# Kernel optimization log

Measured on AMD Instinct MI355X. Metric: run time of the kernel, lower is better.

The kernel has to match this reference:

```python
import jax, jax.numpy as jnp
import numpy as np

S, B, D, V = 1024, 8, 512, 8000


def _ln(x, g, b, eps=1e-5):
    m = x.mean(-1, keepdims=True)
    v = x.var(-1, keepdims=True)
    return (x - m) / jnp.sqrt(v + eps) * g + b


def setup_inputs() -> dict:
    key = jax.random.key(0)
    ks = jax.random.split(key, 8)
    representation = jax.random.normal(ks[0], (S, B, D), jnp.float32)
    # CTC-style logits: tokens come in runs of ~4 frames so argmax has segments
    tok = jax.random.randint(ks[1], (S // 4, B), 0, V)
    tok = jnp.repeat(tok, 4, axis=0)  # [S,B]
    logit = jax.random.normal(ks[2], (S, B, V), jnp.float32) + 6.0 * jax.nn.one_hot(tok, V, dtype=jnp.float32)
    padding = jnp.zeros((B, S), bool)  # all frames valid
    # linear_adapter: Linear(D,2D) -> ReLU -> Linear(2D,D) -> LayerNorm
    w1 = jax.random.normal(ks[3], (2 * D, D), jnp.float32) * (D ** -0.5)
    b1 = jnp.zeros((2 * D,), jnp.float32)
    w2 = jax.random.normal(ks[4], (D, 2 * D), jnp.float32) * ((2 * D) ** -0.5)
    b2 = jnp.zeros((D,), jnp.float32)
    ln1_g = jnp.ones((D,), jnp.float32)
    ln1_b = jnp.zeros((D,), jnp.float32)
    # embed_adapter weight [dict_size, dim], init std = dim**-0.5
    emb_w = jax.random.normal(ks[5], (V, D), jnp.float32) * (D ** -0.5)
    eln_g = jnp.ones((D,), jnp.float32)
    eln_b = jnp.zeros((D,), jnp.float32)
    return dict(representation=representation, logit=logit, padding=padding,
                w1=w1, b1=b1, w2=w2, b2=b2, ln1_g=ln1_g, ln1_b=ln1_b,
                emb_w=emb_w, eln_g=eln_g, eln_b=eln_b)


def reference(representation, logit, padding, w1, b1, w2, b2, ln1_g, ln1_b, emb_w, eln_g, eln_b):
    # distribution = softmax(logit / T), T = 1.0
    dist = jax.nn.softmax(logit, axis=-1)  # [S,B,V]
    # linear adapter: Linear -> ReLU -> Linear -> LN
    h = jax.nn.relu(jnp.einsum('sbd,ed->sbe', representation, w1) + b1)
    linear_out = _ln(jnp.einsum('sbe,de->sbd', h, w2) + b2, ln1_g, ln1_b)
    # context adapter: dist @ embed_adapter.weight, then embed LN
    soft_out = _ln(jnp.einsum('sbv,vd->sbd', dist, emb_w), eln_g, eln_b)
    out = linear_out + soft_out  # league
    # --- CTC 'avg' compress (shrink), vectorized; output padded to S frames ---
    pred = jnp.argmax(dist, axis=-1).T  # [B,S]
    valid = ~padding  # [B,S]
    prev = jnp.concatenate([jnp.full((pred.shape[0], 1), -1, pred.dtype), pred[:, :-1]], axis=1)
    change = (pred != prev) & valid  # segment starts
    seg = jnp.cumsum(change, axis=1) - 1  # segment id per frame
    seg = jnp.where(valid, seg, S)  # invalid frames -> out-of-range id
    # weights_matrix[b, t, s] = 1/len(segment s) if frame t in segment s
    onehot = (seg[:, :, None] == jnp.arange(S)[None, None, :]).astype(out.dtype)  # [B,S,S]
    counts = onehot.sum(1)  # [B,S] frames per segment
    w = onehot * jnp.where(counts > 0, 1.0 / counts, 0.0)[:, None, :]
    # representation.permute(1,2,0).bmm(weights).permute(2,0,1)
    compressed = jnp.einsum('sbd,bst->tbd', out, w)  # [S_new(padded to S), B, D]
    new_lengths = change.sum(1)
    new_padding = jnp.arange(S)[None, :] >= new_lengths[:, None]
    return compressed, new_padding
```

## Files before the change

kernel.cpp:

```cpp
#include <hip/hip_runtime.h>
#include <hip/hip_bf16.h>

typedef __attribute__((ext_vector_type(8))) __bf16 bf16x8;
typedef __attribute__((ext_vector_type(4))) __bf16 bf16x4;
typedef __attribute__((ext_vector_type(4))) float  f32x4;

#define AS1 __attribute__((address_space(1)))
#define AS3 __attribute__((address_space(3)))

__global__ __launch_bounds__(256) void k_cvt(const float* __restrict__ in,
                                             __bf16* __restrict__ out, int n4) {
  int i = blockIdx.x * 256 + threadIdx.x;
  if (i >= n4) return;
  float4 f = reinterpret_cast<const float4*>(in)[i];
  bf16x4 o = { (__bf16)f.x, (__bf16)f.y, (__bf16)f.z, (__bf16)f.w };
  reinterpret_cast<bf16x4*>(out)[i] = o;
}

__global__ __launch_bounds__(256) void k_transpose_cvt(const float* __restrict__ in,
                                                       __bf16* __restrict__ out) {
  __shared__ float t[32][33];
  int bi = blockIdx.x, bj = blockIdx.y;
  int c = threadIdx.x & 31, r8 = threadIdx.x >> 5;
#pragma unroll
  for (int i = 0; i < 4; ++i) {
    int r = r8 + i * 8;
    t[r][c] = in[(size_t)(bi * 32 + r) * 512 + bj * 32 + c];
  }
  __syncthreads();
#pragma unroll
  for (int i = 0; i < 4; ++i) {
    int r = r8 + i * 8;
    out[(size_t)(bj * 32 + r) * 8000 + bi * 32 + c] = (__bf16)t[c][r];
  }
}

__global__ __launch_bounds__(256) void k_softmax(const float* __restrict__ logit,
                                                 __bf16* __restrict__ dist,
                                                 int* __restrict__ pred) {
  int row = blockIdx.x, tid = threadIdx.x;
  int lane = tid & 63, wid = tid >> 6;
  const float4* lr = (const float4*)(logit + (size_t)row * 8000);
  float4 v[8];
  float lmax = -1e30f; int lidx = 0;
#pragma unroll
  for (int j = 0; j < 8; ++j) {
    int i4 = tid + j * 256;
    if (i4 < 2000) v[j] = lr[i4];
    else { v[j].x = v[j].y = v[j].z = v[j].w = -1e30f; }
#pragma unroll
    for (int c = 0; c < 4; ++c) {
      float x = (&v[j].x)[c];
      if (x > lmax) { lmax = x; lidx = i4 * 4 + c; }
    }
  }
#pragma unroll
  for (int o = 32; o; o >>= 1) {
    float ov = __shfl_xor(lmax, o);
    int   oi = __shfl_xor(lidx, o);
    if (ov > lmax || (ov == lmax && oi < lidx)) { lmax = ov; lidx = oi; }
  }
  __shared__ float wmax[4]; __shared__ int widx[4]; __shared__ float wsum[4];
  if (lane == 0) { wmax[wid] = lmax; widx[wid] = lidx; }
  __syncthreads();
  float gmax = wmax[0]; int gidx = widx[0];
#pragma unroll
  for (int w = 1; w < 4; ++w)
    if (wmax[w] > gmax || (wmax[w] == gmax && widx[w] < gidx)) { gmax = wmax[w]; gidx = widx[w]; }
  float ls = 0.f;
#pragma unroll
  for (int j = 0; j < 8; ++j) {
#pragma unroll
    for (int c = 0; c < 4; ++c) {
      float e = __expf((&v[j].x)[c] - gmax);
      (&v[j].x)[c] = e; ls += e;
    }
  }
#pragma unroll
  for (int o = 32; o; o >>= 1) ls += __shfl_xor(ls, o);
  if (lane == 0) wsum[wid] = ls;
  __syncthreads();
  float inv = 1.f / (wsum[0] + wsum[1] + wsum[2] + wsum[3]);
  bf16x4* dr = (bf16x4*)(dist + (size_t)row * 8000);
#pragma unroll
  for (int j = 0; j < 8; ++j) {
    int i4 = tid + j * 256;
    if (i4 < 2000) {
      bf16x4 o = { (__bf16)(v[j].x * inv), (__bf16)(v[j].y * inv),
                   (__bf16)(v[j].z * inv), (__bf16)(v[j].w * inv) };
      dr[i4] = o;
    }
  }
  if (tid == 0) pred[row] = gidx;
}

template<int EPI>
__global__ __launch_bounds__(256) void k_gemm_bt(const __bf16* __restrict__ A,
                                                 const __bf16* __restrict__ B,
                                                 float* __restrict__ Cf,
                                                 __bf16* __restrict__ Cb,
                                                 const float* __restrict__ bias,
                                                 int K, int N, int klen, long long ostride) {
  __shared__ __align__(16) __bf16 lA[2][128 * 64];
  __shared__ __align__(16) __bf16 lB[2][128 * 64];
  int tid = threadIdx.x, lane = tid & 63, wid = tid >> 6;
  int wr = wid >> 1, wc = wid & 1;
  int k0 = blockIdx.z * klen;
  int kn = min(klen, K - k0);
  int nt = kn >> 6;
  const __bf16* Ab = A + (size_t)blockIdx.x * 128 * K + k0;
  const __bf16* Bb = B + (size_t)blockIdx.y * 128 * K + k0;
  int sr = tid >> 3, ss = tid & 7;
  f32x4 acc[4][4] = {};

  auto stage = [&](int buf, int kt) {
#pragma unroll
    for (int i = 0; i < 4; ++i) {
      int r = i * 32 + sr;
      int col = kt + ((ss ^ (r & 7)) << 3);
      __builtin_amdgcn_global_load_lds((const AS1 void*)(Ab + (size_t)r * K + col),
                                       (AS3 void*)(&lA[buf][i * 2048 + tid * 8]), 16, 0, 0);
      __builtin_amdgcn_global_load_lds((const AS1 void*)(Bb + (size_t)r * K + col),
                                       (AS3 void*)(&lB[buf][i * 2048 + tid * 8]), 16, 0, 0);
    }
  };

  stage(0, 0);
  __syncthreads();
  int cur = 0;
  for (int t = 0; t < nt; ++t) {
    if (t + 1 < nt) stage(cur ^ 1, (t + 1) << 6);
#pragma unroll
    for (int kk = 0; kk < 2; ++kk) {
      bf16x8 af[4], bv[4];
#pragma unroll
      for (int m = 0; m < 4; ++m) {
        int r = wr * 64 + m * 16 + (lane & 15);
        int slot = ((kk << 2) + (lane >> 4)) ^ (r & 7);
        af[m] = *(const bf16x8*)((const char*)lA[cur] + r * 128 + slot * 16);
      }
#pragma unroll
      for (int n = 0; n < 4; ++n) {
        int r = wc * 64 + n * 16 + (lane & 15);
        int slot = ((kk << 2) + (lane >> 4)) ^ (r & 7);
        bv[n] = *(const bf16x8*)((const char*)lB[cur] + r * 128 + slot * 16);
      }
#pragma unroll
      for (int m = 0; m < 4; ++m)
#pragma unroll
        for (int n = 0; n < 4; ++n)
          acc[m][n] = __builtin_amdgcn_mfma_f32_16x16x32_bf16(af[m], bv[n], acc[m][n], 0, 0, 0);
    }
    __syncthreads();
    cur ^= 1;
  }
  if (EPI == 0) Cf += (size_t)blockIdx.z * (size_t)ostride;
  int row0 = blockIdx.x * 128 + wr * 64 + ((lane >> 4) << 2);
  int col0 = blockIdx.y * 128 + wc * 64 + (lane & 15);
#pragma unroll
  for (int n = 0; n < 4; ++n) {
    int col = col0 + n * 16;
    float bvv = (EPI >= 1) ? bias[col] : 0.f;
#pragma unroll
    for (int m = 0; m < 4; ++m) {
#pragma unroll
      for (int j = 0; j < 4; ++j) {
        int row = row0 + m * 16 + j;
        float val = acc[m][n][j] + bvv;
        if (EPI == 1) { val = fmaxf(val, 0.f); Cb[(size_t)row * N + col] = (__bf16)val; }
        else          { Cf[(size_t)row * N + col] = val; }
      }
    }
  }
}

__global__ __launch_bounds__(256) void k_lnadd(const float* __restrict__ lin,
                                               const float* __restrict__ s0p,
                                               const float* __restrict__ s1p,
                                               const float* __restrict__ g1, const float* __restrict__ b1,
                                               const float* __restrict__ g2, const float* __restrict__ b2,
                                               float* __restrict__ out) {
  int wid = threadIdx.x >> 6, lane = threadIdx.x & 63;
  int row = blockIdx.x * 4 + wid;
  size_t base = (size_t)row * 512 + lane * 8;
  f32x4 a0 = *(const f32x4*)(lin + base), a1 = *(const f32x4*)(lin + base + 4);
  f32x4 c0 = *(const f32x4*)(s0p + base), c1 = *(const f32x4*)(s0p + base + 4);
  f32x4 d0 = *(const f32x4*)(s1p + base), d1 = *(const f32x4*)(s1p + base + 4);
  float x[8], y[8];
#pragma unroll
  for (int k = 0; k < 4; ++k) {
    x[k] = a0[k]; x[k + 4] = a1[k];
    y[k] = c0[k] + d0[k]; y[k + 4] = c1[k] + d1[k];
  }
  float sx = 0, qx = 0, sy = 0, qy = 0;
#pragma unroll
  for (int k = 0; k < 8; ++k) { sx += x[k]; qx += x[k] * x[k]; sy += y[k]; qy += y[k] * y[k]; }
#pragma unroll
  for (int o = 32; o; o >>= 1) {
    sx += __shfl_xor(sx, o); qx += __shfl_xor(qx, o);
    sy += __shfl_xor(sy, o); qy += __shfl_xor(qy, o);
  }
  const float invD = 1.f / 512.f;
  float mx = sx * invD, vx = qx * invD - mx * mx;
  float my = sy * invD, vy = qy * invD - my * my;
  float rx = rsqrtf(vx + 1e-5f), ry = rsqrtf(vy + 1e-5f);
  float o8[8];
#pragma unroll
  for (int k = 0; k < 8; ++k) {
    int d = lane * 8 + k;
    o8[k] = (x[k] - mx) * rx * g1[d] + b1[d] + (y[k] - my) * ry * g2[d] + b2[d];
  }
  *(f32x4*)(out + base)     = f32x4{o8[0], o8[1], o8[2], o8[3]};
  *(f32x4*)(out + base + 4) = f32x4{o8[4], o8[5], o8[6], o8[7]};
}

__global__ __launch_bounds__(256) void k_scan(const int* __restrict__ pred,
                                              int* __restrict__ seg_start,
                                              int* __restrict__ seg_cnt,
                                              int* __restrict__ new_len,
                                              float* __restrict__ out_pad) {
  __shared__ int lp[8192];
  __shared__ int len_s[8];
  int tid = threadIdx.x;
  for (int i = tid; i < 8192; i += 256) lp[i] = pred[i];
  __syncthreads();
  if (tid < 8) {
    int b = tid, prev = -1, seg = -1, start = 0;
    for (int s = 0; s < 1024; ++s) {
      int p = lp[s * 8 + b];
      if (p != prev) {
        if (seg >= 0) seg_cnt[b * 1024 + seg] = s - start;
        ++seg; seg_start[b * 1024 + seg] = s; start = s; prev = p;
      }
    }
    seg_cnt[b * 1024 + seg] = 1024 - start;
    len_s[b] = seg + 1;
    new_len[b] = seg + 1;
  }
  __syncthreads();
  for (int i = tid; i < 8192; i += 256) {
    int b = i >> 10, s = i & 1023;
    out_pad[b * 1024 + s] = (s >= len_s[b]) ? 1.f : 0.f;
  }
}

__global__ __launch_bounds__(256) void k_compress(const float* __restrict__ outb,
                                                  const int* __restrict__ seg_start,
                                                  const int* __restrict__ seg_cnt,
                                                  const int* __restrict__ new_len,
                                                  float* __restrict__ comp) {
  int wid = threadIdx.x >> 6, lane = threadIdx.x & 63;
  int t = blockIdx.x * 4 + wid, b = blockIdx.y;
  float* dst = comp + ((size_t)(t * 8 + b)) * 512 + lane * 8;
  int len = new_len[b];
  if (t >= len) {
    f32x4 z = {0.f, 0.f, 0.f, 0.f};
    *(f32x4*)dst = z; *(f32x4*)(dst + 4) = z;
    return;
  }
  int s0 = seg_start[b * 1024 + t], cnt = seg_cnt[b * 1024 + t];
  f32x4 a0 = {0.f, 0.f, 0.f, 0.f}, a1 = {0.f, 0.f, 0.f, 0.f};
  for (int s = s0; s < s0 + cnt; ++s) {
    const float* p = outb + ((size_t)(s * 8 + b)) * 512 + lane * 8;
    a0 += *(const f32x4*)p;
    a1 += *(const f32x4*)(p + 4);
  }
  float inv = 1.f / (float)cnt;
  a0 *= inv; a1 *= inv;
  *(f32x4*)dst = a0; *(f32x4*)(dst + 4) = a1;
}

extern "C" void kernel_launch(void* const* d_in, const int* in_sizes, int n_in,
                              void* d_out, int out_size, void* d_ws, size_t ws_size,
                              hipStream_t stream) {
  const float* rep   = (const float*)d_in[0];
  const float* logit = (const float*)d_in[1];
  const float* w1    = (const float*)d_in[3];
  const float* b1    = (const float*)d_in[4];
  const float* w2    = (const float*)d_in[5];
  const float* b2    = (const float*)d_in[6];
  const float* g1    = (const float*)d_in[7];
  const float* bb1   = (const float*)d_in[8];
  const float* emb   = (const float*)d_in[9];
  const float* g2    = (const float*)d_in[10];
  const float* bb2   = (const float*)d_in[11];
  float* out = (float*)d_out;
  (void)in_sizes; (void)n_in; (void)out_size; (void)ws_size;

  char* ws = (char*)d_ws;
  size_t off = 0;
  auto alloc = [&](size_t bytes) -> void* {
    void* p = ws + off; off += (bytes + 255) & ~(size_t)255; return p;
  };
  __bf16* Xb    = (__bf16*)alloc((size_t)8192 * 512 * 2);
  __bf16* w1b   = (__bf16*)alloc((size_t)1024 * 512 * 2);
  __bf16* w2b   = (__bf16*)alloc((size_t)512 * 1024 * 2);
  __bf16* embT  = (__bf16*)alloc((size_t)512 * 8000 * 2);
  __bf16* distb = (__bf16*)alloc((size_t)8192 * 8000 * 2);
  __bf16* Hb    = (__bf16*)alloc((size_t)8192 * 1024 * 2);
  float*  linr  = (float*)alloc((size_t)8192 * 512 * 4);
  float*  sof0  = (float*)alloc((size_t)8192 * 512 * 4 * 2);
  float*  sof1  = sof0 + (size_t)8192 * 512;
  float*  outb  = (float*)alloc((size_t)8192 * 512 * 4);
  int*    pred  = (int*)alloc((size_t)8192 * 4);
  int*    segs  = (int*)alloc((size_t)8192 * 4);
  int*    segc  = (int*)alloc((size_t)8192 * 4);
  int*    nlen  = (int*)alloc(64);

  k_cvt<<<4096, 256, 0, stream>>>(rep, Xb, 1048576);
  k_cvt<<<512, 256, 0, stream>>>(w1, w1b, 131072);
  k_cvt<<<512, 256, 0, stream>>>(w2, w2b, 131072);
  k_transpose_cvt<<<dim3(250, 16), 256, 0, stream>>>(emb, embT);
  k_softmax<<<8192, 256, 0, stream>>>(logit, distb, pred);
  k_gemm_bt<1><<<dim3(64, 8, 1), 256, 0, stream>>>(Xb, w1b, nullptr, Hb, b1, 512, 1024, 512, 0);
  k_gemm_bt<2><<<dim3(64, 4, 1), 256, 0, stream>>>(Hb, w2b, linr, nullptr, b2, 1024, 512, 1024, 0);
  k_gemm_bt<0><<<dim3(64, 4, 2), 256, 0, stream>>>(distb, embT, sof0, nullptr, nullptr,
                                                   8000, 512, 4096, (long long)8192 * 512);
  k_lnadd<<<2048, 256, 0, stream>>>(linr, sof0, sof1, g1, bb1, g2, bb2, outb);
  k_scan<<<1, 256, 0, stream>>>(pred, segs, segc, nlen, out + (size_t)8192 * 512);
  k_compress<<<dim3(256, 8), 256, 0, stream>>>(outb, segs, segc, nlen, out);
}
```

Baseline: 327.1 us.

## Triple-buffer GEMM loads, emit bf16 split-K partials, fuse prep kernels

```diff
diff --git a/kernel.cpp b/kernel.cpp
--- a/kernel.cpp
+++ b/kernel.cpp
@@ -8,30 +8,39 @@
 #define AS1 __attribute__((address_space(1)))
 #define AS3 __attribute__((address_space(3)))
 
-__global__ __launch_bounds__(256) void k_cvt(const float* __restrict__ in,
-                                             __bf16* __restrict__ out, int n4) {
-  int i = blockIdx.x * 256 + threadIdx.x;
-  if (i >= n4) return;
-  float4 f = reinterpret_cast<const float4*>(in)[i];
-  bf16x4 o = { (__bf16)f.x, (__bf16)f.y, (__bf16)f.z, (__bf16)f.w };
-  reinterpret_cast<bf16x4*>(out)[i] = o;
-}
-
-__global__ __launch_bounds__(256) void k_transpose_cvt(const float* __restrict__ in,
-                                                       __bf16* __restrict__ out) {
+__global__ __launch_bounds__(256) void k_prep(const float* __restrict__ rep,
+                                              const float* __restrict__ w1,
+                                              const float* __restrict__ w2,
+                                              const float* __restrict__ emb,
+                                              __bf16* __restrict__ Xb,
+                                              __bf16* __restrict__ w1b,
+                                              __bf16* __restrict__ w2b,
+                                              __bf16* __restrict__ embT) {
   __shared__ float t[32][33];
-  int bi = blockIdx.x, bj = blockIdx.y;
-  int c = threadIdx.x & 31, r8 = threadIdx.x >> 5;
-#pragma unroll
-  for (int i = 0; i < 4; ++i) {
-    int r = r8 + i * 8;
-    t[r][c] = in[(size_t)(bi * 32 + r) * 512 + bj * 32 + c];
-  }
-  __syncthreads();
-#pragma unroll
-  for (int i = 0; i < 4; ++i) {
-    int r = r8 + i * 8;
-    out[(size_t)(bj * 32 + r) * 8000 + bi * 32 + c] = (__bf16)t[c][r];
+  int bid = blockIdx.x;
+  if (bid < 5120) {
+    const float* in; __bf16* out; int i;
+    if (bid < 4096)      { in = rep; out = Xb;  i = bid * 256 + threadIdx.x; }
+    else if (bid < 4608) { in = w1;  out = w1b; i = (bid - 4096) * 256 + threadIdx.x; }
+    else                 { in = w2;  out = w2b; i = (bid - 4608) * 256 + threadIdx.x; }
+    float4 f = reinterpret_cast<const float4*>(in)[i];
+    bf16x4 o = { (__bf16)f.x, (__bf16)f.y, (__bf16)f.z, (__bf16)f.w };
+    reinterpret_cast<bf16x4*>(out)[i] = o;
+  } else {
+    int b2 = bid - 5120;
+    int bi = b2 % 250, bj = b2 / 250;
+    int c = threadIdx.x & 31, r8 = threadIdx.x >> 5;
+#pragma unroll
+    for (int i = 0; i < 4; ++i) {
+      int r = r8 + i * 8;
+      t[r][c] = emb[(size_t)(bi * 32 + r) * 512 + bj * 32 + c];
+    }
+    __syncthreads();
+#pragma unroll
+    for (int i = 0; i < 4; ++i) {
+      int r = r8 + i * 8;
+      embT[(size_t)(bj * 32 + r) * 8000 + bi * 32 + c] = (__bf16)t[c][r];
+    }
   }
 }
 
@@ -97,12 +106,11 @@
 template<int EPI>
 __global__ __launch_bounds__(256) void k_gemm_bt(const __bf16* __restrict__ A,
                                                  const __bf16* __restrict__ B,
-                                                 float* __restrict__ Cf,
                                                  __bf16* __restrict__ Cb,
                                                  const float* __restrict__ bias,
                                                  int K, int N, int klen, long long ostride) {
-  __shared__ __align__(16) __bf16 lA[2][128 * 64];
-  __shared__ __align__(16) __bf16 lB[2][128 * 64];
+  __shared__ __align__(16) __bf16 lA[3][128 * 64];
+  __shared__ __align__(16) __bf16 lB[3][128 * 64];
   int tid = threadIdx.x, lane = tid & 63, wid = tid >> 6;
   int wr = wid >> 1, wc = wid & 1;
   int k0 = blockIdx.z * klen;
@@ -117,7 +125,7 @@
 #pragma unroll
     for (int i = 0; i < 4; ++i) {
       int r = i * 32 + sr;
-      int col = kt + ((ss ^ (r & 7)) << 3);
+      int col = (kt << 6) + ((ss ^ (r & 7)) << 3);
       __builtin_amdgcn_global_load_lds((const AS1 void*)(Ab + (size_t)r * K + col),
                                        (AS3 void*)(&lA[buf][i * 2048 + tid * 8]), 16, 0, 0);
       __builtin_amdgcn_global_load_lds((const AS1 void*)(Bb + (size_t)r * K + col),
@@ -126,10 +134,18 @@
   };
 
   stage(0, 0);
-  __syncthreads();
-  int cur = 0;
+  if (nt > 1) stage(1, 1);
   for (int t = 0; t < nt; ++t) {
-    if (t + 1 < nt) stage(cur ^ 1, (t + 1) << 6);
+    int b = t % 3;
+    if (t + 2 < nt) {
+      stage((t + 2) % 3, t + 2);
+      asm volatile("s_waitcnt vmcnt(16)" ::: "memory");
+    } else if (t + 1 < nt) {
+      asm volatile("s_waitcnt vmcnt(8)" ::: "memory");
+    } else {
+      asm volatile("s_waitcnt vmcnt(0)" ::: "memory");
+    }
+    __builtin_amdgcn_s_barrier();
 #pragma unroll
     for (int kk = 0; kk < 2; ++kk) {
       bf16x8 af[4], bv[4];
@@ -137,13 +153,13 @@
       for (int m = 0; m < 4; ++m) {
         int r = wr * 64 + m * 16 + (lane & 15);
         int slot = ((kk << 2) + (lane >> 4)) ^ (r & 7);
-        af[m] = *(const bf16x8*)((const char*)lA[cur] + r * 128 + slot * 16);
+        af[m] = *(const bf16x8*)((const char*)lA[b] + r * 128 + slot * 16);
       }
 #pragma unroll
       for (int n = 0; n < 4; ++n) {
         int r = wc * 64 + n * 16 + (lane & 15);
         int slot = ((kk << 2) + (lane >> 4)) ^ (r & 7);
-        bv[n] = *(const bf16x8*)((const char*)lB[cur] + r * 128 + slot * 16);
+        bv[n] = *(const bf16x8*)((const char*)lB[b] + r * 128 + slot * 16);
       }
 #pragma unroll
       for (int m = 0; m < 4; ++m)
@@ -151,46 +167,47 @@
         for (int n = 0; n < 4; ++n)
           acc[m][n] = __builtin_amdgcn_mfma_f32_16x16x32_bf16(af[m], bv[n], acc[m][n], 0, 0, 0);
     }
-    __syncthreads();
-    cur ^= 1;
-  }
-  if (EPI == 0) Cf += (size_t)blockIdx.z * (size_t)ostride;
+    __builtin_amdgcn_s_barrier();
+  }
+  if (EPI == 0) Cb += (size_t)blockIdx.z * (size_t)ostride;
   int row0 = blockIdx.x * 128 + wr * 64 + ((lane >> 4) << 2);
   int col0 = blockIdx.y * 128 + wc * 64 + (lane & 15);
 #pragma unroll
   for (int n = 0; n < 4; ++n) {
     int col = col0 + n * 16;
-    float bvv = (EPI >= 1) ? bias[col] : 0.f;
+    float bvv = (EPI == 1) ? bias[col] : 0.f;
 #pragma unroll
     for (int m = 0; m < 4; ++m) {
 #pragma unroll
       for (int j = 0; j < 4; ++j) {
         int row = row0 + m * 16 + j;
         float val = acc[m][n][j] + bvv;
-        if (EPI == 1) { val = fmaxf(val, 0.f); Cb[(size_t)row * N + col] = (__bf16)val; }
-        else          { Cf[(size_t)row * N + col] = val; }
+        if (EPI == 1) val = fmaxf(val, 0.f);
+        Cb[(size_t)row * N + col] = (__bf16)val;
       }
     }
   }
 }
 
-__global__ __launch_bounds__(256) void k_lnadd(const float* __restrict__ lin,
-                                               const float* __restrict__ s0p,
-                                               const float* __restrict__ s1p,
+__global__ __launch_bounds__(256) void k_lnadd(const __bf16* __restrict__ lin,
+                                               const __bf16* __restrict__ sof,
+                                               const float* __restrict__ bias2,
                                                const float* __restrict__ g1, const float* __restrict__ b1,
                                                const float* __restrict__ g2, const float* __restrict__ b2,
                                                float* __restrict__ out) {
+  const long long P = (long long)8192 * 512;
   int wid = threadIdx.x >> 6, lane = threadIdx.x & 63;
   int row = blockIdx.x * 4 + wid;
   size_t base = (size_t)row * 512 + lane * 8;
-  f32x4 a0 = *(const f32x4*)(lin + base), a1 = *(const f32x4*)(lin + base + 4);
-  f32x4 c0 = *(const f32x4*)(s0p + base), c1 = *(const f32x4*)(s0p + base + 4);
-  f32x4 d0 = *(const f32x4*)(s1p + base), d1 = *(const f32x4*)(s1p + base + 4);
+  bf16x8 l0 = *(const bf16x8*)(lin + base);
+  bf16x8 l1 = *(const bf16x8*)(lin + P + base);
+  bf16x8 s0 = *(const bf16x8*)(sof + base);
+  bf16x8 s1 = *(const bf16x8*)(sof + P + base);
   float x[8], y[8];
 #pragma unroll
-  for (int k = 0; k < 4; ++k) {
-    x[k] = a0[k]; x[k + 4] = a1[k];
-    y[k] = c0[k] + d0[k]; y[k + 4] = c1[k] + d1[k];
+  for (int k = 0; k < 8; ++k) {
+    x[k] = (float)l0[k] + (float)l1[k] + bias2[lane * 8 + k];
+    y[k] = (float)s0[k] + (float)s1[k];
   }
   float sx = 0, qx = 0, sy = 0, qy = 0;
 #pragma unroll
@@ -222,12 +239,13 @@
   __shared__ int lp[8192];
   __shared__ int len_s[8];
   int tid = threadIdx.x;
-  for (int i = tid; i < 8192; i += 256) lp[i] = pred[i];
+  for (int i = tid; i < 8192; i += 256) lp[(i & 7) * 1024 + (i >> 3)] = pred[i];
   __syncthreads();
   if (tid < 8) {
     int b = tid, prev = -1, seg = -1, start = 0;
+    const int* row = lp + b * 1024;
     for (int s = 0; s < 1024; ++s) {
-      int p = lp[s * 8 + b];
+      int p = row[s];
       if (p != prev) {
         if (seg >= 0) seg_cnt[b * 1024 + seg] = s - start;
         ++seg; seg_start[b * 1024 + seg] = s; start = s; prev = p;
@@ -292,31 +310,27 @@
   auto alloc = [&](size_t bytes) -> void* {
     void* p = ws + off; off += (bytes + 255) & ~(size_t)255; return p;
   };
-  __bf16* Xb    = (__bf16*)alloc((size_t)8192 * 512 * 2);
+  const long long P = (long long)8192 * 512;
+  __bf16* Xb    = (__bf16*)alloc((size_t)P * 2);
   __bf16* w1b   = (__bf16*)alloc((size_t)1024 * 512 * 2);
   __bf16* w2b   = (__bf16*)alloc((size_t)512 * 1024 * 2);
   __bf16* embT  = (__bf16*)alloc((size_t)512 * 8000 * 2);
   __bf16* distb = (__bf16*)alloc((size_t)8192 * 8000 * 2);
   __bf16* Hb    = (__bf16*)alloc((size_t)8192 * 1024 * 2);
-  float*  linr  = (float*)alloc((size_t)8192 * 512 * 4);
-  float*  sof0  = (float*)alloc((size_t)8192 * 512 * 4 * 2);
-  float*  sof1  = sof0 + (size_t)8192 * 512;
-  float*  outb  = (float*)alloc((size_t)8192 * 512 * 4);
+  __bf16* linp  = (__bf16*)alloc((size_t)P * 2 * 2);
+  __bf16* sofp  = (__bf16*)alloc((size_t)P * 2 * 2);
+  float*  outb  = (float*)alloc((size_t)P * 4);
   int*    pred  = (int*)alloc((size_t)8192 * 4);
   int*    segs  = (int*)alloc((size_t)8192 * 4);
   int*    segc  = (int*)alloc((size_t)8192 * 4);
   int*    nlen  = (int*)alloc(64);
 
-  k_cvt<<<4096, 256, 0, stream>>>(rep, Xb, 1048576);
-  k_cvt<<<512, 256, 0, stream>>>(w1, w1b, 131072);
-  k_cvt<<<512, 256, 0, stream>>>(w2, w2b, 131072);
-  k_transpose_cvt<<<dim3(250, 16), 256, 0, stream>>>(emb, embT);
+  k_prep<<<9120, 256, 0, stream>>>(rep, w1, w2, emb, Xb, w1b, w2b, embT);
   k_softmax<<<8192, 256, 0, stream>>>(logit, distb, pred);
-  k_gemm_bt<1><<<dim3(64, 8, 1), 256, 0, stream>>>(Xb, w1b, nullptr, Hb, b1, 512, 1024, 512, 0);
-  k_gemm_bt<2><<<dim3(64, 4, 1), 256, 0, stream>>>(Hb, w2b, linr, nullptr, b2, 1024, 512, 1024, 0);
-  k_gemm_bt<0><<<dim3(64, 4, 2), 256, 0, stream>>>(distb, embT, sof0, nullptr, nullptr,
-                                                   8000, 512, 4096, (long long)8192 * 512);
-  k_lnadd<<<2048, 256, 0, stream>>>(linr, sof0, sof1, g1, bb1, g2, bb2, outb);
+  k_gemm_bt<1><<<dim3(64, 8, 1), 256, 0, stream>>>(Xb, w1b, Hb, b1, 512, 1024, 512, 0);
+  k_gemm_bt<0><<<dim3(64, 4, 2), 256, 0, stream>>>(Hb, w2b, linp, nullptr, 1024, 512, 512, P);
+  k_gemm_bt<0><<<dim3(64, 4, 2), 256, 0, stream>>>(distb, embT, sofp, nullptr, 8000, 512, 4032, P);
+  k_lnadd<<<2048, 256, 0, stream>>>(linp, sofp, b2, g1, bb1, g2, bb2, outb);
   k_scan<<<1, 256, 0, stream>>>(pred, segs, segc, nlen, out + (size_t)8192 * 512);
   k_compress<<<dim3(256, 8), 256, 0, stream>>>(outb, segs, segc, nlen, out);
 }
```

After: 400.9 us. 22.6% more time.
